# Performance work log

Measured on AMD Instinct MI355X. Metric: run time of the kernel, lower is better.

## Reference

```python
import jax, jax.numpy as jnp
import numpy as np


def setup_inputs() -> dict:
    key = jax.random.key(0)
    ks = jax.random.split(key, 7)
    B, T, K, H, A = 32, 32, 196, 512, 512
    # Xavier-normal-ish scale for square 512x512 linears
    s = float(np.sqrt(2.0 / (H + A)))
    return {
        "att_feats": jax.random.normal(ks[0], (B, K, H), jnp.float32),
        "hiddens": jax.random.normal(ks[1], (B, T, H), jnp.float32),
        "sentinel": jax.random.normal(ks[2], (B, T, H), jnp.float32),
        "Wv": jax.random.normal(ks[3], (H, A), jnp.float32) * s,
        "Wg": jax.random.normal(ks[4], (H, A), jnp.float32) * s,
        "Ws": jax.random.normal(ks[5], (H, A), jnp.float32) * s,
        "wh": jax.random.normal(ks[6], (A,), jnp.float32) * s,
    }


def reference(att_feats, hiddens, sentinel, Wv, Wg, Ws, wh):
    # Dropout treated as identity (eval mode / deterministic reference).
    cv = jnp.einsum("bkh,ha->bka", att_feats, Wv)          # [B,K,A]
    cg = jnp.einsum("bth,ha->bta", hiddens, Wg)            # [B,T,A]
    # Broadcast additive attention: [B,T,K,A]
    content_v = cv[:, None, :, :] + cg[:, :, None, :]
    z_t = jnp.einsum("btka,a->btk", jnp.tanh(content_v), wh)  # [B,T,K]
    alpha_t = jax.nn.softmax(z_t, axis=-1)                    # [B,T,K]
    c_t = jnp.einsum("btk,bkh->bth", alpha_t, att_feats)      # [B,T,H]
    # Sentinel branch
    content_s = jnp.einsum("bth,ha->bta", sentinel, Ws) + cg  # [B,T,A]
    z_ext = jnp.einsum("bta,a->bt", jnp.tanh(content_s), wh)[..., None]  # [B,T,1]
    extended = jnp.concatenate([z_t, z_ext], axis=2)          # [B,T,K+1]
    alpha_hat = jax.nn.softmax(extended, axis=-1)
    beta_t = alpha_hat[:, :, -1:]                             # [B,T,1]
    c_hat_t = beta_t * sentinel + (1.0 - beta_t) * c_t        # [B,T,H]
    return (c_hat_t, alpha_t, beta_t)
```

## Files before the change

### kernel.cpp

```cpp
#include <hip/hip_runtime.h>
#include <hip/hip_bf16.h>
#include <math.h>

#define HDIM 512
#define ADIM 512
#define BATCH 32
#define TDIM 32
#define KDIM 196
#define MROWS 8320
#define ZSC 2.885390081777927f

typedef short short8 __attribute__((ext_vector_type(8)));
typedef float floatx4 __attribute__((ext_vector_type(4)));

__device__ __forceinline__ void gl_lds16(const __hip_bfloat16* g, __hip_bfloat16* l) {
    __builtin_amdgcn_global_load_lds(
        (const __attribute__((address_space(1))) unsigned int*)(const void*)g,
        (__attribute__((address_space(3))) unsigned int*)(void*)l, 16, 0, 0);
}

__device__ __forceinline__ float tanh_ps(float up) {
    float e = __builtin_amdgcn_exp2f(up);
    float r = __builtin_amdgcn_rcpf(e + 1.0f);
    return fmaf(-2.0f, r, 1.0f);
}

__global__ __launch_bounds__(256) void conv_fused(const float* __restrict__ att,
                                                  const float* __restrict__ hid,
                                                  const float* __restrict__ sen,
                                                  const float* __restrict__ Wv,
                                                  const float* __restrict__ Wg,
                                                  const float* __restrict__ Ws,
                                                  __hip_bfloat16* __restrict__ ahi,
                                                  __hip_bfloat16* __restrict__ alo,
                                                  __hip_bfloat16* __restrict__ bthi,
                                                  __hip_bfloat16* __restrict__ btlo) {
    __shared__ float tile[64][65];
    const int tid = threadIdx.x;

    if (blockIdx.x < 4160) {
        const int idx = blockIdx.x * 256 + tid;
        const int row = idx >> 7;
        float4 v;
        if (row < 6272)      v = ((const float4*)att)[idx];
        else if (row < 7296) v = ((const float4*)hid)[idx - 6272 * 128];
        else                 v = ((const float4*)sen)[idx - 7296 * 128];
        float x[4] = {v.x, v.y, v.z, v.w};
        union { __hip_bfloat16 b[4]; uint2 u; } H, L;
        #pragma unroll
        for (int i = 0; i < 4; ++i) {
            H.b[i] = __float2bfloat16(x[i]);
            L.b[i] = __float2bfloat16(x[i] - __bfloat162float(H.b[i]));
        }
        ((uint2*)ahi)[idx] = H.u;
        ((uint2*)alo)[idx] = L.u;
    } else {
        const int bid = blockIdx.x - 4160;
        const int mz  = bid >> 6;
        const int rem = bid & 63;
        const int k0  = (rem >> 3) * 64;
        const int n0  = (rem & 7) * 64;
        const float* src = mz == 0 ? Wv : (mz == 1 ? Wg : Ws);
        #pragma unroll
        for (int i = 0; i < 16; ++i) {
            int k = (tid >> 6) * 16 + i;
            int n = tid & 63;
            tile[k][n] = src[(size_t)(k0 + k) * 512 + n0 + n];
        }
        __syncthreads();
        const size_t obase = (size_t)mz * 262144;
        #pragma unroll
        for (int i = 0; i < 16; ++i) {
            int n = (tid >> 6) * 16 + i;
            int k = tid & 63;
            float x = tile[k][n];
            __hip_bfloat16 h = __float2bfloat16(x);
            __hip_bfloat16 l = __float2bfloat16(x - __bfloat162float(h));
            size_t o = obase + (size_t)(n0 + n) * 512 + k0 + k;
            bthi[o] = h;
            btlo[o] = l;
        }
    }
}

__global__ __launch_bounds__(256) void gemm_bf16x3(
        const __hip_bfloat16* __restrict__ Ahi, const __hip_bfloat16* __restrict__ Alo,
        const __hip_bfloat16* __restrict__ Bthi, const __hip_bfloat16* __restrict__ Btlo,
        float* __restrict__ C) {
    __shared__ __hip_bfloat16 smem[12288];

    const int tid  = threadIdx.x;
    const int lane = tid & 63;
    const int wave = tid >> 6;
    const int wm = wave >> 1;
    const int wn = wave & 1;
    const int row0 = blockIdx.x * 64;
    const int col0 = blockIdx.y * 128;
    const int seg = (row0 < 6272) ? 0 : ((row0 < 7296) ? 1 : 2);
    const __hip_bfloat16* Bh = Bthi + (size_t)seg * 262144;
    const __hip_bfloat16* Bl = Btlo + (size_t)seg * 262144;

    floatx4 acc[2][4];
    #pragma unroll
    for (int i = 0; i < 2; ++i)
        #pragma unroll
        for (int j = 0; j < 4; ++j)
            acc[i][j] = (floatx4){0.f, 0.f, 0.f, 0.f};

    const int kq8 = (lane >> 4) << 3;

    for (int k0 = 0; k0 < 512; k0 += 32) {
        #pragma unroll
        for (int s = 0; s < 6; ++s) {
            int u = tid + (s << 8);
            __hip_bfloat16* ldst = smem + u * 8;
            const __hip_bfloat16* gsrc;
            if (u < 256)        gsrc = Ahi + (size_t)(row0 + (u >> 2)) * 512 + k0 + ((u & 3) << 3);
            else if (u < 512)   { int v = u - 256;  gsrc = Alo + (size_t)(row0 + (v >> 2)) * 512 + k0 + ((v & 3) << 3); }
            else if (u < 1024)  { int v = u - 512;  gsrc = Bh  + (size_t)(col0 + (v >> 2)) * 512 + k0 + ((v & 3) << 3); }
            else                { int v = u - 1024; gsrc = Bl  + (size_t)(col0 + (v >> 2)) * 512 + k0 + ((v & 3) << 3); }
            gl_lds16(gsrc, ldst);
        }
        asm volatile("s_waitcnt vmcnt(0)" ::: "memory");
        __syncthreads();

        short8 a_hi[2], a_lo[2], b_hi[4], b_lo[4];
        #pragma unroll
        for (int i = 0; i < 2; ++i) {
            int m = wm * 32 + i * 16 + (lane & 15);
            a_hi[i] = *(const short8*)(smem + m * 32 + kq8);
            a_lo[i] = *(const short8*)(smem + 2048 + m * 32 + kq8);
        }
        #pragma unroll
        for (int j = 0; j < 4; ++j) {
            int n = wn * 64 + j * 16 + (lane & 15);
            b_hi[j] = *(const short8*)(smem + 4096 + n * 32 + kq8);
            b_lo[j] = *(const short8*)(smem + 8192 + n * 32 + kq8);
        }

        #pragma unroll
        for (int i = 0; i < 2; ++i)
            #pragma unroll
            for (int j = 0; j < 4; ++j) {
                acc[i][j] = __builtin_amdgcn_mfma_f32_16x16x32_bf16(a_hi[i], b_hi[j], acc[i][j], 0, 0, 0);
                acc[i][j] = __builtin_amdgcn_mfma_f32_16x16x32_bf16(a_hi[i], b_lo[j], acc[i][j], 0, 0, 0);
                acc[i][j] = __builtin_amdgcn_mfma_f32_16x16x32_bf16(a_lo[i], b_hi[j], acc[i][j], 0, 0, 0);
            }
        __syncthreads();
    }

    #pragma unroll
    for (int i = 0; i < 2; ++i) {
        #pragma unroll
        for (int r = 0; r < 4; ++r) {
            int row = row0 + wm * 32 + i * 16 + ((lane >> 4) << 2) + r;
            float* cp = C + (size_t)row * 512 + col0 + wn * 64 + (lane & 15);
            #pragma unroll
            for (int j = 0; j < 4; ++j) cp[j * 16] = acc[i][j][r] * ZSC;
        }
    }
}

__global__ __launch_bounds__(256) void z_kernel(const float* __restrict__ cv,
                                                const float* __restrict__ cg,
                                                const float* __restrict__ wh,
                                                float* __restrict__ z_t) {
    __shared__ float cvs[8][132];
    __shared__ float cgs[32][132];
    __shared__ float whs[132];

    const int kb  = blockIdx.x;
    const int b   = blockIdx.y;
    const int tid = threadIdx.x;
    const int t       = tid & 31;
    const int k_local = tid >> 5;
    const int k       = kb * 8 + k_local;
    const bool do_z = (k < KDIM);

    const int r_st = tid >> 5;
    const int q_st = tid & 31;

    float acc = 0.f, acc2 = 0.f;

    for (int c = 0; c < 4; ++c) {
        const int a0 = c * 128;
        __syncthreads();
        {
            int kr = kb * 8 + r_st;
            if (kr < KDIM)
                *(float4*)&cvs[r_st][4 * q_st] =
                    *(const float4*)(cv + ((size_t)b * KDIM + kr) * ADIM + a0 + 4 * q_st);
        }
        #pragma unroll
        for (int s = 0; s < 4; ++s) {
            int idx = tid + s * 256;
            int rr = idx >> 5, qq = idx & 31;
            *(float4*)&cgs[rr][4 * qq] =
                *(const float4*)(cg + ((size_t)b * TDIM + rr) * ADIM + a0 + 4 * qq);
        }
        if (tid < 32)
            *(float4*)&whs[4 * tid] = *(const float4*)(wh + a0 + 4 * tid);
        __syncthreads();

        if (do_z) {
            #pragma unroll 8
            for (int q = 0; q < 32; ++q) {
                float4 v  = *(const float4*)&cvs[k_local][4 * q];
                float4 g  = *(const float4*)&cgs[t][4 * q];
                float4 w4 = *(const float4*)&whs[4 * q];
                acc  = fmaf(w4.x, tanh_ps(v.x + g.x), acc);
                acc2 = fmaf(w4.y, tanh_ps(v.y + g.y), acc2);
                acc  = fmaf(w4.z, tanh_ps(v.z + g.z), acc);
                acc2 = fmaf(w4.w, tanh_ps(v.w + g.w), acc2);
            }
        }
    }

    if (do_z) z_t[((size_t)b * TDIM + t) * KDIM + k] = acc + acc2;
}

__global__ __launch_bounds__(256) void out_kernel(const float* __restrict__ z_t,
                                                  const float* __restrict__ cs,
                                                  const float* __restrict__ cg,
                                                  const float* __restrict__ wh,
                                                  const float* __restrict__ att,
                                                  const float* __restrict__ sen,
                                                  float* __restrict__ out_chat,
                                                  float* __restrict__ out_alpha,
                                                  float* __restrict__ out_beta) {
    __shared__ float alpha_s[4][200];
    __shared__ float beta_s[4];

    const int tg = blockIdx.x;
    const int b  = blockIdx.y;
    const int tid  = threadIdx.x;
    const int wave = tid >> 6;
    const int lane = tid & 63;
    const int t = tg * 4 + wave;

    const float* csrow = cs + ((size_t)b * TDIM + t) * ADIM;
    const float* cgrow = cg + ((size_t)b * TDIM + t) * ADIM;
    float p = 0.f;
    #pragma unroll
    for (int h = 0; h < 2; ++h) {
        float4 sv = *(const float4*)(csrow + 8 * lane + 4 * h);
        float4 gv = *(const float4*)(cgrow + 8 * lane + 4 * h);
        float4 w4 = *(const float4*)(wh + 8 * lane + 4 * h);
        p = fmaf(w4.x, tanh_ps(sv.x + gv.x), p);
        p = fmaf(w4.y, tanh_ps(sv.y + gv.y), p);
        p = fmaf(w4.z, tanh_ps(sv.z + gv.z), p);
        p = fmaf(w4.w, tanh_ps(sv.w + gv.w), p);
    }
    #pragma unroll
    for (int off = 32; off; off >>= 1) p += __shfl_xor(p, off, 64);
    const float se = p;

    const float* zrow = z_t + ((size_t)b * TDIM + t) * KDIM;
    float z0 = zrow[lane];
    float z1 = zrow[lane + 64];
    float z2 = zrow[lane + 128];
    float z3 = (lane < 4) ? zrow[lane + 192] : -INFINITY;

    float m = fmaxf(fmaxf(z0, z1), fmaxf(z2, z3));
    #pragma unroll
    for (int off = 32; off; off >>= 1) m = fmaxf(m, __shfl_xor(m, off, 64));

    float e0 = __expf(z0 - m), e1 = __expf(z1 - m);
    float e2 = __expf(z2 - m), e3 = (lane < 4) ? __expf(z3 - m) : 0.0f;
    float s = e0 + e1 + e2 + e3;
    #pragma unroll
    for (int off = 32; off; off >>= 1) s += __shfl_xor(s, off, 64);

    float invS = 1.0f / s;
    float a0 = e0 * invS, a1 = e1 * invS, a2 = e2 * invS, a3 = e3 * invS;

    float* arow = out_alpha + ((size_t)b * TDIM + t) * KDIM;
    alpha_s[wave][lane] = a0;        arow[lane] = a0;
    alpha_s[wave][lane + 64] = a1;   arow[lane + 64] = a1;
    alpha_s[wave][lane + 128] = a2;  arow[lane + 128] = a2;
    if (lane < 4) { alpha_s[wave][lane + 192] = a3; arow[lane + 192] = a3; }

    float m2 = fmaxf(m, se);
    float eext = __expf(se - m2);
    float S2 = s * __expf(m - m2) + eext;
    float beta = eext / S2;
    if (lane == 0) {
        beta_s[wave] = beta;
        out_beta[b * TDIM + t] = beta;
    }
    __syncthreads();

    const float* attb = att + (size_t)b * KDIM * HDIM;
    float acc[4][2] = {};
    #pragma unroll 4
    for (int k = 0; k < KDIM; ++k) {
        float av0 = attb[(size_t)k * HDIM + tid];
        float av1 = attb[(size_t)k * HDIM + tid + 256];
        #pragma unroll
        for (int w = 0; w < 4; ++w) {
            float a = alpha_s[w][k];
            acc[w][0] = fmaf(a, av0, acc[w][0]);
            acc[w][1] = fmaf(a, av1, acc[w][1]);
        }
    }

    #pragma unroll
    for (int w = 0; w < 4; ++w) {
        int tt = tg * 4 + w;
        float bt = beta_s[w];
        float om = 1.0f - bt;
        size_t o = ((size_t)b * TDIM + tt) * HDIM;
        out_chat[o + tid]       = fmaf(bt, sen[o + tid],       om * acc[w][0]);
        out_chat[o + tid + 256] = fmaf(bt, sen[o + tid + 256], om * acc[w][1]);
    }
}

__global__ __launch_bounds__(256) void gemm_f32(const float* __restrict__ Amat,
                                                const float* __restrict__ Bmat,
                                                float* __restrict__ Cmat) {
    __shared__ float As[16][64 + 4];
    __shared__ float Bs[16][64];
    const int tid = threadIdx.x;
    const int tx = tid & 15;
    const int ty = tid >> 4;
    const int row0 = blockIdx.x * 64;
    const int col0 = blockIdx.y * 64;
    float acc[4][4] = {};
    for (int k0 = 0; k0 < HDIM; k0 += 16) {
        #pragma unroll
        for (int i = 0; i < 4; ++i) {
            int idx = tid + i * 256;
            As[idx & 15][idx >> 4] = Amat[(size_t)(row0 + (idx >> 4)) * HDIM + k0 + (idx & 15)];
        }
        #pragma unroll
        for (int i = 0; i < 4; ++i) {
            int idx = tid + i * 256;
            Bs[idx >> 6][idx & 63] = Bmat[(size_t)(k0 + (idx >> 6)) * ADIM + col0 + (idx & 63)];
        }
        __syncthreads();
        #pragma unroll
        for (int k = 0; k < 16; ++k) {
            float4 a4 = *(const float4*)&As[k][ty * 4];
            float4 b4 = *(const float4*)&Bs[k][tx * 4];
            float a[4] = {a4.x, a4.y, a4.z, a4.w};
            float b[4] = {b4.x, b4.y, b4.z, b4.w};
            #pragma unroll
            for (int i = 0; i < 4; ++i)
                #pragma unroll
                for (int j = 0; j < 4; ++j)
                    acc[i][j] += a[i] * b[j];
        }
        __syncthreads();
    }
    #pragma unroll
    for (int i = 0; i < 4; ++i) {
        size_t r = (size_t)(row0 + ty * 4 + i) * ADIM + col0 + tx * 4;
        #pragma unroll
        for (int j = 0; j < 4; ++j) Cmat[r + j] = acc[i][j] * ZSC;
    }
}

extern "C" void kernel_launch(void* const* d_in, const int* in_sizes, int n_in,
                              void* d_out, int out_size, void* d_ws, size_t ws_size,
                              hipStream_t stream) {
    const float* att = (const float*)d_in[0];
    const float* hid = (const float*)d_in[1];
    const float* sen = (const float*)d_in[2];
    const float* Wv  = (const float*)d_in[3];
    const float* Wg  = (const float*)d_in[4];
    const float* Ws  = (const float*)d_in[5];
    const float* wh  = (const float*)d_in[6];

    float* out = (float*)d_out;
    float* out_chat  = out;
    float* out_alpha = out + 524288;
    float* out_beta  = out + 524288 + 200704;

    char* wsb = (char*)d_ws;
    const size_t C_BYTES  = (size_t)MROWS * 512 * 4;
    const size_t ZT_BYTES = 200704 * 4;
    const size_t AH_BYTES = (size_t)MROWS * 512 * 2;
    const size_t BT_BYTES = (size_t)3 * 512 * 512 * 2;
    const size_t need = C_BYTES + ZT_BYTES + 2 * AH_BYTES + 2 * BT_BYTES;

    float* C  = (float*)wsb;
    float* cv = C;
    float* cg = C + 6272 * 512;
    float* cs = C + 7296 * 512;
    float* zt = (float*)(wsb + C_BYTES);

    if (ws_size >= need) {
        __hip_bfloat16* ahi  = (__hip_bfloat16*)(wsb + C_BYTES + ZT_BYTES);
        __hip_bfloat16* alo  = ahi + (size_t)MROWS * 512;
        __hip_bfloat16* bthi = alo + (size_t)MROWS * 512;
        __hip_bfloat16* btlo = bthi + (size_t)3 * 512 * 512;

        conv_fused<<<4352, 256, 0, stream>>>(att, hid, sen, Wv, Wg, Ws,
                                             ahi, alo, bthi, btlo);
        gemm_bf16x3<<<dim3(130, 4), 256, 0, stream>>>(ahi, alo, bthi, btlo, C);
    } else {
        gemm_f32<<<dim3(98, 8), 256, 0, stream>>>(att, Wv, cv);
        gemm_f32<<<dim3(16, 8), 256, 0, stream>>>(hid, Wg, cg);
        gemm_f32<<<dim3(16, 8), 256, 0, stream>>>(sen, Ws, cs);
    }

    z_kernel<<<dim3(25, 32), 256, 0, stream>>>(cv, cg, wh, zt);

    out_kernel<<<dim3(8, 32), 256, 0, stream>>>(zt, cs, cg, wh, att, sen,
                                                out_chat, out_alpha, out_beta);
}
```

Baseline: 161.4 us.

## Fuse activation bf16 hi/lo split into GEMM A-tile load

Removes the separate pass that converted att/hid/sen into bf16 hi/lo workspace arrays. The GEMM now loads fp32 A rows directly, splits them into hi/lo in registers and writes them to LDS, while B tiles still come in through async global-to-LDS loads. This drops a full write and re-read of the activation arrays and the extra workspace, at the cost of redoing the conversion in each of the 4 column blocks and issuing synchronous A loads.

Measured after the change: 149.9 us. 7.1% less time.

```diff
diff --git a/kernel.cpp b/kernel.cpp
--- a/kernel.cpp
+++ b/kernel.cpp
@@ -25,66 +25,43 @@
     return fmaf(-2.0f, r, 1.0f);
 }
 
-__global__ __launch_bounds__(256) void conv_fused(const float* __restrict__ att,
-                                                  const float* __restrict__ hid,
-                                                  const float* __restrict__ sen,
-                                                  const float* __restrict__ Wv,
-                                                  const float* __restrict__ Wg,
-                                                  const float* __restrict__ Ws,
-                                                  __hip_bfloat16* __restrict__ ahi,
-                                                  __hip_bfloat16* __restrict__ alo,
-                                                  __hip_bfloat16* __restrict__ bthi,
-                                                  __hip_bfloat16* __restrict__ btlo) {
+__global__ __launch_bounds__(256) void convB(const float* __restrict__ Wv,
+                                             const float* __restrict__ Wg,
+                                             const float* __restrict__ Ws,
+                                             __hip_bfloat16* __restrict__ bthi,
+                                             __hip_bfloat16* __restrict__ btlo) {
     __shared__ float tile[64][65];
     const int tid = threadIdx.x;
-
-    if (blockIdx.x < 4160) {
-        const int idx = blockIdx.x * 256 + tid;
-        const int row = idx >> 7;
-        float4 v;
-        if (row < 6272)      v = ((const float4*)att)[idx];
-        else if (row < 7296) v = ((const float4*)hid)[idx - 6272 * 128];
-        else                 v = ((const float4*)sen)[idx - 7296 * 128];
-        float x[4] = {v.x, v.y, v.z, v.w};
-        union { __hip_bfloat16 b[4]; uint2 u; } H, L;
-        #pragma unroll
-        for (int i = 0; i < 4; ++i) {
-            H.b[i] = __float2bfloat16(x[i]);
-            L.b[i] = __float2bfloat16(x[i] - __bfloat162float(H.b[i]));
-        }
-        ((uint2*)ahi)[idx] = H.u;
-        ((uint2*)alo)[idx] = L.u;
-    } else {
-        const int bid = blockIdx.x - 4160;
-        const int mz  = bid >> 6;
-        const int rem = bid & 63;
-        const int k0  = (rem >> 3) * 64;
-        const int n0  = (rem & 7) * 64;
-        const float* src = mz == 0 ? Wv : (mz == 1 ? Wg : Ws);
-        #pragma unroll
-        for (int i = 0; i < 16; ++i) {
-            int k = (tid >> 6) * 16 + i;
-            int n = tid & 63;
-            tile[k][n] = src[(size_t)(k0 + k) * 512 + n0 + n];
-        }
-        __syncthreads();
-        const size_t obase = (size_t)mz * 262144;
-        #pragma unroll
-        for (int i = 0; i < 16; ++i) {
-            int n = (tid >> 6) * 16 + i;
-            int k = tid & 63;
-            float x = tile[k][n];
-            __hip_bfloat16 h = __float2bfloat16(x);
-            __hip_bfloat16 l = __float2bfloat16(x - __bfloat162float(h));
-            size_t o = obase + (size_t)(n0 + n) * 512 + k0 + k;
-            bthi[o] = h;
-            btlo[o] = l;
-        }
+    const int bid = blockIdx.x;
+    const int mz  = bid >> 6;
+    const int rem = bid & 63;
+    const int k0  = (rem >> 3) * 64;
+    const int n0  = (rem & 7) * 64;
+    const float* src = mz == 0 ? Wv : (mz == 1 ? Wg : Ws);
+    #pragma unroll
+    for (int i = 0; i < 16; ++i) {
+        int k = (tid >> 6) * 16 + i;
+        int n = tid & 63;
+        tile[k][n] = src[(size_t)(k0 + k) * 512 + n0 + n];
+    }
+    __syncthreads();
+    const size_t obase = (size_t)mz * 262144;
+    #pragma unroll
+    for (int i = 0; i < 16; ++i) {
+        int n = (tid >> 6) * 16 + i;
+        int k = tid & 63;
+        float x = tile[k][n];
+        __hip_bfloat16 h = __float2bfloat16(x);
+        __hip_bfloat16 l = __float2bfloat16(x - __bfloat162float(h));
+        size_t o = obase + (size_t)(n0 + n) * 512 + k0 + k;
+        bthi[o] = h;
+        btlo[o] = l;
     }
 }
 
 __global__ __launch_bounds__(256) void gemm_bf16x3(
-        const __hip_bfloat16* __restrict__ Ahi, const __hip_bfloat16* __restrict__ Alo,
+        const float* __restrict__ att, const float* __restrict__ hid,
+        const float* __restrict__ sen,
         const __hip_bfloat16* __restrict__ Bthi, const __hip_bfloat16* __restrict__ Btlo,
         float* __restrict__ C) {
     __shared__ __hip_bfloat16 smem[12288];
@@ -97,6 +74,8 @@
     const int row0 = blockIdx.x * 64;
     const int col0 = blockIdx.y * 128;
     const int seg = (row0 < 6272) ? 0 : ((row0 < 7296) ? 1 : 2);
+    const float* Asrc = seg == 0 ? att : (seg == 1 ? hid : sen);
+    const int arow0 = row0 - (seg == 0 ? 0 : (seg == 1 ? 6272 : 7296));
     const __hip_bfloat16* Bh = Bthi + (size_t)seg * 262144;
     const __hip_bfloat16* Bl = Btlo + (size_t)seg * 262144;
 
@@ -108,18 +87,35 @@
             acc[i][j] = (floatx4){0.f, 0.f, 0.f, 0.f};
 
     const int kq8 = (lane >> 4) << 3;
+    const int a_row = tid >> 2;
+    const int a_k   = (tid & 3) << 3;
 
     for (int k0 = 0; k0 < 512; k0 += 32) {
         #pragma unroll
-        for (int s = 0; s < 6; ++s) {
+        for (int s = 0; s < 4; ++s) {
             int u = tid + (s << 8);
-            __hip_bfloat16* ldst = smem + u * 8;
-            const __hip_bfloat16* gsrc;
-            if (u < 256)        gsrc = Ahi + (size_t)(row0 + (u >> 2)) * 512 + k0 + ((u & 3) << 3);
-            else if (u < 512)   { int v = u - 256;  gsrc = Alo + (size_t)(row0 + (v >> 2)) * 512 + k0 + ((v & 3) << 3); }
-            else if (u < 1024)  { int v = u - 512;  gsrc = Bh  + (size_t)(col0 + (v >> 2)) * 512 + k0 + ((v & 3) << 3); }
-            else                { int v = u - 1024; gsrc = Bl  + (size_t)(col0 + (v >> 2)) * 512 + k0 + ((v & 3) << 3); }
-            gl_lds16(gsrc, ldst);
+            if (u < 512) {
+                gl_lds16(Bh + (size_t)(col0 + (u >> 2)) * 512 + k0 + ((u & 3) << 3),
+                         smem + 4096 + u * 8);
+            } else {
+                int v = u - 512;
+                gl_lds16(Bl + (size_t)(col0 + (v >> 2)) * 512 + k0 + ((v & 3) << 3),
+                         smem + 8192 + v * 8);
+            }
+        }
+        {
+            const float* ap = Asrc + (size_t)(arow0 + a_row) * 512 + k0 + a_k;
+            float4 v0 = *(const float4*)ap;
+            float4 v1 = *(const float4*)(ap + 4);
+            float x[8] = {v0.x, v0.y, v0.z, v0.w, v1.x, v1.y, v1.z, v1.w};
+            union { __hip_bfloat16 h[8]; short8 v; } Hi, Lo;
+            #pragma unroll
+            for (int i = 0; i < 8; ++i) {
+                Hi.h[i] = __float2bfloat16(x[i]);
+                Lo.h[i] = __float2bfloat16(x[i] - __bfloat162float(Hi.h[i]));
+            }
+            *(short8*)(smem + a_row * 32 + a_k)        = Hi.v;
+            *(short8*)(smem + 2048 + a_row * 32 + a_k) = Lo.v;
         }
         asm volatile("s_waitcnt vmcnt(0)" ::: "memory");
         __syncthreads();
@@ -379,9 +375,8 @@
     char* wsb = (char*)d_ws;
     const size_t C_BYTES  = (size_t)MROWS * 512 * 4;
     const size_t ZT_BYTES = 200704 * 4;
-    const size_t AH_BYTES = (size_t)MROWS * 512 * 2;
     const size_t BT_BYTES = (size_t)3 * 512 * 512 * 2;
-    const size_t need = C_BYTES + ZT_BYTES + 2 * AH_BYTES + 2 * BT_BYTES;
+    const size_t need = C_BYTES + ZT_BYTES + 2 * BT_BYTES;
 
     float* C  = (float*)wsb;
     float* cv = C;
@@ -390,14 +385,11 @@
     float* zt = (float*)(wsb + C_BYTES);
 
     if (ws_size >= need) {
-        __hip_bfloat16* ahi  = (__hip_bfloat16*)(wsb + C_BYTES + ZT_BYTES);
-        __hip_bfloat16* alo  = ahi + (size_t)MROWS * 512;
-        __hip_bfloat16* bthi = alo + (size_t)MROWS * 512;
+        __hip_bfloat16* bthi = (__hip_bfloat16*)(wsb + C_BYTES + ZT_BYTES);
         __hip_bfloat16* btlo = bthi + (size_t)3 * 512 * 512;
 
-        conv_fused<<<4352, 256, 0, stream>>>(att, hid, sen, Wv, Wg, Ws,
-                                             ahi, alo, bthi, btlo);
-        gemm_bf16x3<<<dim3(130, 4), 256, 0, stream>>>(ahi, alo, bthi, btlo, C);
+        convB<<<192, 256, 0, stream>>>(Wv, Wg, Ws, bthi, btlo);
+        gemm_bf16x3<<<dim3(130, 4), 256, 0, stream>>>(att, hid, sen, bthi, btlo, C);
     } else {
         gemm_f32<<<dim3(98, 8), 256, 0, stream>>>(att, Wv, cv);
         gemm_f32<<<dim3(16, 8), 256, 0, stream>>>(hid, Wg, cg);
```
